# Kernel optimization log

Measured on AMD Instinct MI355X. Metric: run time of the kernel, lower is better.

Reference implementation:

```python
import jax, jax.numpy as jnp
import numpy as np

N, E, B, DIM, NF, EF, HID = 50000, 100000, 2000, 64, 14, 4, 128


def setup_inputs() -> dict:
    key = jax.random.key(0)
    ks = jax.random.split(key, 30)
    rn = lambda k, shape, scale: jax.random.normal(k, shape, jnp.float32) * scale
    inp = {}
    inp["x"] = rn(ks[0], (N, NF), 1.0)
    inp["edge_attr"] = jax.random.uniform(ks[1], (E, EF), jnp.float32)
    inp["edge_index"] = jax.random.randint(ks[2], (2, E), 0, N)
    # equal-size graphs: 25 nodes per graph, sorted segment ids
    inp["batch"] = (jnp.arange(N, dtype=jnp.int32) // (N // B)).astype(jnp.int32)
    inp["lin0_w"] = rn(ks[3], (DIM, NF), (1.0 / NF) ** 0.5)
    inp["lin0_b"] = jnp.zeros((DIM,), jnp.float32)
    inp["mlp_w1"] = rn(ks[4], (HID, EF), (1.0 / EF) ** 0.5)
    inp["mlp_b1"] = jnp.zeros((HID,), jnp.float32)
    inp["mlp_w2"] = rn(ks[5], (DIM * DIM, HID), (1.0 / HID) ** 0.5)
    inp["mlp_b2"] = jnp.zeros((DIM * DIM,), jnp.float32)
    inp["root"] = rn(ks[6], (DIM, DIM), (1.0 / DIM) ** 0.5)
    inp["conv_b"] = jnp.zeros((DIM,), jnp.float32)
    inp["gru_wih"] = rn(ks[7], (3 * DIM, DIM), (1.0 / DIM) ** 0.5)
    inp["gru_whh"] = rn(ks[8], (3 * DIM, DIM), (1.0 / DIM) ** 0.5)
    inp["gru_bih"] = jnp.zeros((3 * DIM,), jnp.float32)
    inp["gru_bhh"] = jnp.zeros((3 * DIM,), jnp.float32)
    inp["lstm_wih"] = rn(ks[9], (4 * DIM, 2 * DIM), (1.0 / (2 * DIM)) ** 0.5)
    inp["lstm_whh"] = rn(ks[10], (4 * DIM, DIM), (1.0 / DIM) ** 0.5)
    inp["lstm_bih"] = jnp.zeros((4 * DIM,), jnp.float32)
    inp["lstm_bhh"] = jnp.zeros((4 * DIM,), jnp.float32)
    inp["lin1_w"] = rn(ks[11], (DIM, 2 * DIM), (1.0 / (2 * DIM)) ** 0.5)
    inp["lin1_b"] = jnp.zeros((DIM,), jnp.float32)
    inp["lin2_w"] = rn(ks[12], (1, DIM), (1.0 / DIM) ** 0.5)
    inp["lin2_b"] = jnp.zeros((1,), jnp.float32)
    return inp


def _forward(x, edge_attr, edge_index, batch, lin0_w, lin0_b, mlp_w1, mlp_b1,
             mlp_w2, mlp_b2, root, conv_b, gru_wih, gru_whh, gru_bih, gru_bhh,
             lstm_wih, lstm_whh, lstm_bih, lstm_bhh, lin1_w, lin1_b, lin2_w, lin2_b):
    src, dst = edge_index[0], edge_index[1]
    n = x.shape[0]
    # edge MLP -> per-edge weight matrices [E, DIM, DIM]
    h_e = jax.nn.relu(edge_attr @ mlp_w1.T + mlp_b1)
    W_e = (h_e @ mlp_w2.T + mlp_b2).reshape(-1, DIM, DIM)
    deg = jnp.clip(jax.ops.segment_sum(jnp.ones_like(dst, jnp.float32), dst, n), 1.0)

    out = jax.nn.relu(x @ lin0_w.T + lin0_b)
    h = out  # GRU hidden (seq_len=1, 1 layer)
    for _ in range(3):
        msg = jnp.einsum('ei,eio->eo', out[src], W_e)  # per-edge matmul
        agg = jax.ops.segment_sum(msg, dst, n) / deg[:, None]  # scatter-mean
        m = jax.nn.relu(agg + out @ root + conv_b)  # NNConv: aggr + root + bias
        # GRU step
        gi = m @ gru_wih.T + gru_bih
        gh = h @ gru_whh.T + gru_bhh
        i_r, i_z, i_n = jnp.split(gi, 3, axis=-1)
        h_r, h_z, h_n = jnp.split(gh, 3, axis=-1)
        r = jax.nn.sigmoid(i_r + h_r)
        z = jax.nn.sigmoid(i_z + h_z)
        ng = jnp.tanh(i_n + r * h_n)
        h = (1.0 - z) * ng + z * h
        out = h

    # Set2Set pooling, 3 processing steps
    b = B
    qh = jnp.zeros((b, DIM), out.dtype)
    qc = jnp.zeros((b, DIM), out.dtype)
    q_star = jnp.zeros((b, 2 * DIM), out.dtype)
    for _ in range(3):
        gates = q_star @ lstm_wih.T + lstm_bih + qh @ lstm_whh.T + lstm_bhh
        gi_, gf_, gg_, go_ = jnp.split(gates, 4, axis=-1)
        qc = jax.nn.sigmoid(gf_) * qc + jax.nn.sigmoid(gi_) * jnp.tanh(gg_)
        qh = jax.nn.sigmoid(go_) * jnp.tanh(qc)
        q = qh
        e = jnp.sum(out * q[batch], axis=-1)  # [N]
        e_max = jax.ops.segment_max(e, batch, b)
        a = jnp.exp(e - e_max[batch])
        denom = jax.ops.segment_sum(a, batch, b)
        a = a / denom[batch]
        r_read = jax.ops.segment_sum(a[:, None] * out, batch, b)
        q_star = jnp.concatenate([q, r_read], axis=-1)

    y = jax.nn.relu(q_star @ lin1_w.T + lin1_b)
    y = y @ lin2_w.T + lin2_b
    return y.reshape(-1)


def reference(x, edge_attr, edge_index, batch, lin0_w, lin0_b, mlp_w1, mlp_b1,
              mlp_w2, mlp_b2, root, conv_b, gru_wih, gru_whh, gru_bih, gru_bhh,
              lstm_wih, lstm_whh, lstm_bih, lstm_bhh, lin1_w, lin1_b, lin2_w, lin2_b):
    return _forward(x, edge_attr, edge_index, batch, lin0_w, lin0_b, mlp_w1, mlp_b1,
                    mlp_w2, mlp_b2, root, conv_b, gru_wih, gru_whh, gru_bih, gru_bhh,
                    lstm_wih, lstm_whh, lstm_bih, lstm_bhh, lin1_w, lin1_b, lin2_w, lin2_b)
```

## Files before the change

kernel.cpp:

```cpp
#include <hip/hip_runtime.h>
#include <hip/hip_bf16.h>

#define NN 50000
#define EE 100000
#define BB 2000
#define DIM 64
#define NF 14
#define EF 4
#define HID 128
#define EPAD 100096

typedef __attribute__((ext_vector_type(8))) _Float16 half8;
typedef __attribute__((ext_vector_type(4))) _Float16 half4;
typedef __attribute__((ext_vector_type(4))) float floatx4;

__global__ void transpose_kernel(const float* __restrict__ lih, const float* __restrict__ lhh,
                                 const float* __restrict__ l1,
                                 float* __restrict__ lihT, float* __restrict__ lhhT,
                                 float* __restrict__ l1T) {
    int t = blockIdx.x * 256 + threadIdx.x;
    if (t < 256 * 128) { int j = t / 128, k = t % 128; lihT[k * 256 + j] = lih[t]; }
    if (t < 256 * 64) { int j = t / 64, k = t % 64; lhhT[k * 256 + j] = lhh[t]; }
    if (t < 64 * 128) { int d = t / 128, k = t % 128; l1T[k * 64 + d] = l1[t]; }
}

__global__ void prep_gru_kernel(const float* __restrict__ root, const float* __restrict__ b2,
                                const float* __restrict__ wih, const float* __restrict__ whh,
                                const float* __restrict__ bih, const float* __restrict__ bhh,
                                _Float16* __restrict__ W1h, _Float16* __restrict__ W2h,
                                float* __restrict__ fbias) {
    int t = blockIdx.x * 256 + threadIdx.x;
    if (t < 64 * 128) {
        int n = t >> 7, k = t & 127;
        W1h[t] = (_Float16)(k < 64 ? root[k * 64 + n] : b2[(size_t)(k - 64) * 64 + n]);
    }
    if (t < 256 * 128) {
        int n2 = t >> 7, k = t & 127;
        int g = n2 >> 6, j = n2 & 63;
        float v;
        if (g == 0)      v = (k < 64) ? wih[j * 64 + k]         : whh[j * 64 + (k - 64)];
        else if (g == 1) v = (k < 64) ? wih[(64 + j) * 64 + k]  : whh[(64 + j) * 64 + (k - 64)];
        else if (g == 2) v = (k < 64) ? wih[(128 + j) * 64 + k] : 0.f;
        else             v = (k < 64) ? 0.f                     : whh[(128 + j) * 64 + (k - 64)];
        W2h[t] = (_Float16)v;
    }
    if (t < 256) {
        int g = t >> 6, j = t & 63;
        float v = (g == 0) ? bih[j] + bhh[j]
                : (g == 1) ? bih[64 + j] + bhh[64 + j]
                : (g == 2) ? bih[128 + j] : bhh[128 + j];
        fbias[t] = v;
    }
}

__global__ void lin0_kernel(const float* __restrict__ x, const float* __restrict__ w,
                            const float* __restrict__ b, float* __restrict__ hv) {
    int t = blockIdx.x * 256 + threadIdx.x;
    if (t >= NN * 64) return;
    int n = t >> 6, d = t & 63;
    float acc = b[d];
    #pragma unroll
    for (int f = 0; f < NF; f++) acc += x[n * NF + f] * w[d * NF + f];
    hv[t] = fmaxf(acc, 0.f);
}

__global__ void deg_kernel(const int* __restrict__ ei, float* __restrict__ deg) {
    int e = blockIdx.x * 256 + threadIdx.x;
    if (e < EE) atomicAdd(&deg[ei[EE + e]], 1.0f);
}

__global__ void he16_kernel(const float* __restrict__ ea, const float* __restrict__ w1,
                            const float* __restrict__ b1, _Float16* __restrict__ he) {
    int t = blockIdx.x * 256 + threadIdx.x;
    if (t >= EPAD * 128) return;
    int el = t >> 7, h = t & 127;
    float acc = 0.f;
    if (el < EE) {
        const float4 a = *(const float4*)(ea + (size_t)el * 4);
        const float4 w = *(const float4*)(w1 + h * 4);
        acc = fmaxf(b1[h] + a.x * w.x + a.y * w.y + a.z * w.z + a.w * w.w, 0.f);
    }
    he[t] = (_Float16)acc;
}

__global__ void w2rt_kernel(const float* __restrict__ w2, _Float16* __restrict__ W2rT) {
    int t = blockIdx.x * 256 + threadIdx.x;
    if (t >= 64 * 8192) return;
    int o = t >> 13, k = t & 8191, i = k >> 7, h = k & 127;
    W2rT[(size_t)o * 8192 + k] = (_Float16)w2[(size_t)(i * 64 + o) * 128 + h];
}

__global__ __launch_bounds__(256, 2) void msg_gemm_kernel(
    const float* __restrict__ hv, const _Float16* __restrict__ he16,
    const _Float16* __restrict__ W2rT, const int* __restrict__ ei,
    float* __restrict__ agg, float* __restrict__ xsum) {
    __shared__ _Float16 sB[2][16 * 64 * 8];
    __shared__ _Float16 sXs[256 * 68];
    __shared__ int sDst[256];
    const int t = threadIdx.x;
    const int eb = blockIdx.x * 256;
    const int lane = t & 63;
    const int w = t >> 6;
    const int col = lane & 15;
    const int quad = lane >> 4;

    if (t < 256) {
        int e = eb + t;
        sDst[t] = (e < EE) ? ei[EE + e] : 0;
    }
    #pragma unroll 4
    for (int rep = 0; rep < 16; rep++) {
        int idx = rep * 256 + t;
        int el = idx >> 4, d4 = idx & 15;
        int e = eb + el;
        float4 v = {0.f, 0.f, 0.f, 0.f};
        if (e < EE) {
            int src = ei[e];
            v = *(const float4*)(hv + (size_t)src * 64 + d4 * 4);
        }
        half4 h4 = {(_Float16)v.x, (_Float16)v.y, (_Float16)v.z, (_Float16)v.w};
        *(half4*)&sXs[el * 68 + d4 * 4] = h4;
    }

    half8 heReg[4][4];
    #pragma unroll
    for (int mt = 0; mt < 4; mt++) {
        int row = eb + w * 64 + mt * 16 + col;
        #pragma unroll
        for (int p = 0; p < 4; p++)
            heReg[mt][p] = *(const half8*)(he16 + (size_t)row * 128 + p * 32 + quad * 8);
    }

    floatx4 Cacc[4][4];
    #pragma unroll
    for (int mt = 0; mt < 4; mt++)
        #pragma unroll
        for (int nt = 0; nt < 4; nt++)
            Cacc[mt][nt] = (floatx4){0.f, 0.f, 0.f, 0.f};

    const size_t gbase = (size_t)(w * 16 + col) * 8192 + quad * 8;
    half8 pre[4];
    {
        #pragma unroll
        for (int rep = 0; rep < 4; rep++)
            pre[rep] = *(const half8*)(W2rT + gbase + 0 * 128 + rep * 32);
        #pragma unroll
        for (int rep = 0; rep < 4; rep++)
            *(half8*)&sB[0][((w * 4 + rep) * 64 + lane) * 8] = pre[rep];
    }
    __syncthreads();

    #pragma unroll 1
    for (int i = 0; i < 64; i++) {
        int buf = i & 1;
        if (i < 63) {
            #pragma unroll
            for (int rep = 0; rep < 4; rep++)
                pre[rep] = *(const half8*)(W2rT + gbase + (size_t)(i + 1) * 128 + rep * 32);
        }
        _Float16 xsx[4];
        #pragma unroll
        for (int mt = 0; mt < 4; mt++)
            xsx[mt] = sXs[(w * 64 + mt * 16 + col) * 68 + i];
        #pragma unroll
        for (int ks = 0; ks < 4; ks++) {
            half8 bfr[4];
            #pragma unroll
            for (int nt = 0; nt < 4; nt++)
                bfr[nt] = *(const half8*)&sB[buf][((nt * 4 + ks) * 64 + lane) * 8];
            #pragma unroll
            for (int mt = 0; mt < 4; mt++) {
                half8 afr = heReg[mt][ks] * xsx[mt];
                #pragma unroll
                for (int nt = 0; nt < 4; nt++)
                    Cacc[mt][nt] = __builtin_amdgcn_mfma_f32_16x16x32_f16(afr, bfr[nt], Cacc[mt][nt], 0, 0, 0);
            }
        }
        if (i < 63) {
            #pragma unroll
            for (int rep = 0; rep < 4; rep++)
                *(half8*)&sB[buf ^ 1][((w * 4 + rep) * 64 + lane) * 8] = pre[rep];
        }
        __syncthreads();
    }

    #pragma unroll
    for (int mt = 0; mt < 4; mt++) {
        #pragma unroll
        for (int r = 0; r < 4; r++) {
            int el = w * 64 + mt * 16 + quad * 4 + r;
            if (eb + el < EE) {
                float* ap = agg + (size_t)sDst[el] * 64 + col;
                #pragma unroll
                for (int nt = 0; nt < 4; nt++)
                    atomicAdd(ap + nt * 16, Cacc[mt][nt][r]);
            }
        }
    }
    #pragma unroll 4
    for (int rep = 0; rep < 64; rep++) {
        int idx = rep * 256 + t;
        int el = idx >> 6, d = idx & 63;
        if (eb + el < EE)
            atomicAdd(&xsum[(size_t)sDst[el] * 64 + d], (float)sXs[el * 68 + d]);
    }
}

__global__ __launch_bounds__(256, 2) void node_fused_kernel(
    const float* __restrict__ hv_in, float* __restrict__ agg,
    float* __restrict__ xsum, const float* __restrict__ deg,
    const _Float16* __restrict__ W1h, const _Float16* __restrict__ W2h,
    const float* __restrict__ fbias, const float* __restrict__ cb,
    float* __restrict__ hv_out) {
    __shared__ _Float16 sA1[64 * 136];
    __shared__ _Float16 sA2[64 * 136];
    __shared__ float sH[64 * 68];
    __shared__ float sAgg[64 * 68];
    const int t = threadIdx.x;
    const int nb = blockIdx.x * 64;
    const int n = t >> 2, part = t & 3;
    {
        int gn = nb + n;
        bool valid = gn < NN;
        float inv = 1.f;
        if (valid) inv = 1.f / fmaxf(deg[gn], 1.f);
        #pragma unroll
        for (int c4 = 0; c4 < 4; c4++) {
            int d0 = part * 16 + c4 * 4;
            float4 hvv = {0.f, 0.f, 0.f, 0.f}, agv = {0.f, 0.f, 0.f, 0.f}, xsv = {0.f, 0.f, 0.f, 0.f};
            if (valid) {
                hvv = *(const float4*)(hv_in + (size_t)gn * 64 + d0);
                agv = *(const float4*)(agg + (size_t)gn * 64 + d0);
                xsv = *(const float4*)(xsum + (size_t)gn * 64 + d0);
            }
            agv.x *= inv; agv.y *= inv; agv.z *= inv; agv.w *= inv;
            xsv.x *= inv; xsv.y *= inv; xsv.z *= inv; xsv.w *= inv;
            half4 hvh = {(_Float16)hvv.x, (_Float16)hvv.y, (_Float16)hvv.z, (_Float16)hvv.w};
            half4 xsh = {(_Float16)xsv.x, (_Float16)xsv.y, (_Float16)xsv.z, (_Float16)xsv.w};
            *(half4*)&sA1[n * 136 + d0] = hvh;
            *(half4*)&sA1[n * 136 + 64 + d0] = xsh;
            *(half4*)&sA2[n * 136 + 64 + d0] = hvh;
            *(float4*)&sH[n * 68 + d0] = hvv;
            *(float4*)&sAgg[n * 68 + d0] = agv;
        }
        if (valid) {
            float4 z = {0.f, 0.f, 0.f, 0.f};
            #pragma unroll
            for (int c4 = 0; c4 < 4; c4++) {
                int d0 = part * 16 + c4 * 4;
                *(float4*)(agg + (size_t)gn * 64 + d0) = z;
                *(float4*)(xsum + (size_t)gn * 64 + d0) = z;
            }
        }
    }
    __syncthreads();

    const int lane = t & 63, w = t >> 6;
    const int col = lane & 15, quad = lane >> 4;

    floatx4 C1[4];
    #pragma unroll
    for (int nt = 0; nt < 4; nt++) {
        float b = cb[nt * 16 + col];
        C1[nt] = (floatx4){b, b, b, b};
    }
    #pragma unroll
    for (int ks = 0; ks < 4; ks++) {
        half8 a = *(const half8*)&sA1[(w * 16 + col) * 136 + ks * 32 + quad * 8];
        #pragma unroll
        for (int nt = 0; nt < 4; nt++) {
            half8 bfr = *(const half8*)(W1h + (size_t)(nt * 16 + col) * 128 + ks * 32 + quad * 8);
            C1[nt] = __builtin_amdgcn_mfma_f32_16x16x32_f16(a, bfr, C1[nt], 0, 0, 0);
        }
    }
    #pragma unroll
    for (int nt = 0; nt < 4; nt++) {
        #pragma unroll
        for (int r = 0; r < 4; r++) {
            int node = w * 16 + quad * 4 + r;
            int j = nt * 16 + col;
            float m = fmaxf(C1[nt][r] + sAgg[node * 68 + j], 0.f);
            sA2[node * 136 + j] = (_Float16)m;
        }
    }
    __syncthreads();

    floatx4 C2[16];
    #pragma unroll
    for (int nt2 = 0; nt2 < 16; nt2++) {
        float b = fbias[nt2 * 16 + col];
        C2[nt2] = (floatx4){b, b, b, b};
    }
    #pragma unroll
    for (int ks = 0; ks < 4; ks++) {
        half8 a = *(const half8*)&sA2[(w * 16 + col) * 136 + ks * 32 + quad * 8];
        #pragma unroll
        for (int nt2 = 0; nt2 < 16; nt2++) {
            half8 bfr = *(const half8*)(W2h + (size_t)(nt2 * 16 + col) * 128 + ks * 32 + quad * 8);
            C2[nt2] = __builtin_amdgcn_mfma_f32_16x16x32_f16(a, bfr, C2[nt2], 0, 0, 0);
        }
    }
    float hnew[4][4];
    #pragma unroll
    for (int r = 0; r < 4; r++) {
        int node = w * 16 + quad * 4 + r;
        #pragma unroll
        for (int jt = 0; jt < 4; jt++) {
            int j = jt * 16 + col;
            float rr = 1.f / (1.f + expf(-C2[jt][r]));
            float zz = 1.f / (1.f + expf(-C2[4 + jt][r]));
            float ng = tanhf(C2[8 + jt][r] + rr * C2[12 + jt][r]);
            float hold = sH[node * 68 + j];
            hnew[r][jt] = (1.f - zz) * ng + zz * hold;
        }
    }
    __syncthreads();
    #pragma unroll
    for (int r = 0; r < 4; r++) {
        int node = w * 16 + quad * 4 + r;
        #pragma unroll
        for (int jt = 0; jt < 4; jt++)
            sH[node * 68 + jt * 16 + col] = hnew[r][jt];
    }
    __syncthreads();
    {
        int gn = nb + n;
        if (gn < NN) {
            #pragma unroll
            for (int c4 = 0; c4 < 4; c4++) {
                int d0 = part * 16 + c4 * 4;
                *(float4*)(hv_out + (size_t)gn * 64 + d0) = *(const float4*)&sH[n * 68 + d0];
            }
        }
    }
}

__global__ __launch_bounds__(256) void set2set_kernel(
    const float* __restrict__ hv,
    const float* __restrict__ lihT, const float* __restrict__ lhhT,
    const float* __restrict__ l_bih, const float* __restrict__ l_bhh,
    const float* __restrict__ lin1T, const float* __restrict__ lin1_b,
    const float* __restrict__ lin2_w, const float* __restrict__ lin2_b,
    float* __restrict__ out) {
    __shared__ float outS[25 * 65];
    __shared__ float qs[128], qh[64], qc[64], gat[256], ew[32], aw[32], red[64];
    int g = blockIdx.x;
    int t = threadIdx.x;
    for (int p = t; p < 25 * 64; p += 256) {
        int j = p >> 6, i = p & 63;
        outS[j * 65 + i] = hv[(size_t)(g * 25 + j) * 64 + i];
    }
    if (t < 128) qs[t] = 0.f;
    if (t < 64) { qh[t] = 0.f; qc[t] = 0.f; }
    __syncthreads();
    for (int it = 0; it < 3; it++) {
        float acc = l_bih[t] + l_bhh[t];
        for (int k = 0; k < 128; k++) acc += qs[k] * lihT[k * 256 + t];
        for (int k = 0; k < 64; k++) acc += qh[k] * lhhT[k * 256 + t];
        gat[t] = acc;
        __syncthreads();
        if (t < 64) {
            float ig = 1.f / (1.f + expf(-gat[t]));
            float fg = 1.f / (1.f + expf(-gat[64 + t]));
            float gg = tanhf(gat[128 + t]);
            float og = 1.f / (1.f + expf(-gat[192 + t]));
            float c = fg * qc[t] + ig * gg;
            qc[t] = c;
            qh[t] = og * tanhf(c);
        }
        __syncthreads();
        if (t < 25) {
            float e = 0.f;
            for (int i = 0; i < 64; i++) e += outS[t * 65 + i] * qh[i];
            ew[t] = e;
        }
        __syncthreads();
        if (t == 0) {
            float mx = ew[0];
            for (int j = 1; j < 25; j++) mx = fmaxf(mx, ew[j]);
            float s = 0.f;
            for (int j = 0; j < 25; j++) { float a = expf(ew[j] - mx); aw[j] = a; s += a; }
            float inv = 1.f / s;
            for (int j = 0; j < 25; j++) aw[j] *= inv;
        }
        __syncthreads();
        if (t < 64) {
            float r = 0.f;
            for (int j = 0; j < 25; j++) r += aw[j] * outS[j * 65 + t];
            qs[t] = qh[t];
            qs[64 + t] = r;
        }
        __syncthreads();
    }
    if (t < 64) {
        float y1 = lin1_b[t];
        for (int k = 0; k < 128; k++) y1 += qs[k] * lin1T[k * 64 + t];
        y1 = fmaxf(y1, 0.f);
        red[t] = y1 * lin2_w[t];
    }
    __syncthreads();
    if (t == 0) {
        float y = lin2_b[0];
        for (int i = 0; i < 64; i++) y += red[i];
        out[g] = y;
    }
}

extern "C" void kernel_launch(void* const* d_in, const int* in_sizes, int n_in,
                              void* d_out, int out_size, void* d_ws, size_t ws_size,
                              hipStream_t stream) {
    const float* x        = (const float*)d_in[0];
    const float* ea       = (const float*)d_in[1];
    const int*   ei       = (const int*)  d_in[2];
    const float* lin0_w   = (const float*)d_in[4];
    const float* lin0_b   = (const float*)d_in[5];
    const float* mlp_w1   = (const float*)d_in[6];
    const float* mlp_b1   = (const float*)d_in[7];
    const float* mlp_w2   = (const float*)d_in[8];
    const float* mlp_b2   = (const float*)d_in[9];
    const float* root     = (const float*)d_in[10];
    const float* conv_b   = (const float*)d_in[11];
    const float* gru_wih  = (const float*)d_in[12];
    const float* gru_whh  = (const float*)d_in[13];
    const float* gru_bih  = (const float*)d_in[14];
    const float* gru_bhh  = (const float*)d_in[15];
    const float* lstm_wih = (const float*)d_in[16];
    const float* lstm_whh = (const float*)d_in[17];
    const float* lstm_bih = (const float*)d_in[18];
    const float* lstm_bhh = (const float*)d_in[19];
    const float* lin1_w   = (const float*)d_in[20];
    const float* lin1_b   = (const float*)d_in[21];
    const float* lin2_w   = (const float*)d_in[22];
    const float* lin2_b   = (const float*)d_in[23];
    float* out = (float*)d_out;

    char* base = (char*)d_ws;
    size_t off = 0;
    auto carve = [&](size_t bytes) -> void* {
        void* r = base + off;
        off = (off + bytes + 255) & ~(size_t)255;
        return r;
    };
    float* hv   = (float*)carve((size_t)NN * 64 * 4);
    float* agg  = (float*)carve((size_t)NN * 64 * 4);
    float* xsum = (float*)carve((size_t)NN * 64 * 4);
    float* deg  = (float*)carve((size_t)NN * 4);
    float* lihT = (float*)carve(128 * 256 * 4);
    float* lhhT = (float*)carve(64 * 256 * 4);
    float* l1T  = (float*)carve(128 * 64 * 4);
    float* fbias = (float*)carve(256 * 4);
    _Float16* he16 = (_Float16*)carve((size_t)EPAD * 128 * 2);
    _Float16* W2rT = (_Float16*)carve((size_t)64 * 8192 * 2);
    _Float16* W1h  = (_Float16*)carve((size_t)64 * 128 * 2);
    _Float16* W2h  = (_Float16*)carve((size_t)256 * 128 * 2);

    hipMemsetAsync(deg, 0, (size_t)NN * 4, stream);
    hipMemsetAsync(agg, 0, (size_t)NN * 64 * 4 * 2, stream);
    transpose_kernel<<<128, 256, 0, stream>>>(lstm_wih, lstm_whh, lin1_w, lihT, lhhT, l1T);
    prep_gru_kernel<<<128, 256, 0, stream>>>(root, mlp_b2, gru_wih, gru_whh, gru_bih, gru_bhh,
                                             W1h, W2h, fbias);
    lin0_kernel<<<(NN * 64 + 255) / 256, 256, 0, stream>>>(x, lin0_w, lin0_b, hv);
    deg_kernel<<<(EE + 255) / 256, 256, 0, stream>>>(ei, deg);
    he16_kernel<<<(EPAD * 128 + 255) / 256, 256, 0, stream>>>(ea, mlp_w1, mlp_b1, he16);
    w2rt_kernel<<<(64 * 8192 + 255) / 256, 256, 0, stream>>>(mlp_w2, W2rT);

    for (int it = 0; it < 3; it++) {
        msg_gemm_kernel<<<EPAD / 256, 256, 0, stream>>>(hv, he16, W2rT, ei, agg, xsum);
        node_fused_kernel<<<(NN + 63) / 64, 256, 0, stream>>>(hv, agg, xsum, deg,
                                                              W1h, W2h, fbias, conv_b, hv);
    }

    set2set_kernel<<<BB, 256, 0, stream>>>(hv, lihT, lhhT, lstm_bih, lstm_bhh,
                                           l1T, lin1_b, lin2_w, lin2_b, out);
}
```

Before: 763.8 us.

## Retile message GEMM to 64-edge blocks with register-streamed W2 operands

```diff
diff --git a/kernel.cpp b/kernel.cpp
--- a/kernel.cpp
+++ b/kernel.cpp
@@ -90,27 +90,26 @@
     W2rT[(size_t)o * 8192 + k] = (_Float16)w2[(size_t)(i * 64 + o) * 128 + h];
 }
 
-__global__ __launch_bounds__(256, 2) void msg_gemm_kernel(
+__global__ __launch_bounds__(128, 2) void msg_gemm_kernel(
     const float* __restrict__ hv, const _Float16* __restrict__ he16,
     const _Float16* __restrict__ W2rT, const int* __restrict__ ei,
     float* __restrict__ agg, float* __restrict__ xsum) {
-    __shared__ _Float16 sB[2][16 * 64 * 8];
-    __shared__ _Float16 sXs[256 * 68];
-    __shared__ int sDst[256];
+    __shared__ _Float16 sXs[64 * 68];
+    __shared__ int sDst[64];
     const int t = threadIdx.x;
-    const int eb = blockIdx.x * 256;
+    const int eb = blockIdx.x * 64;
     const int lane = t & 63;
     const int w = t >> 6;
     const int col = lane & 15;
     const int quad = lane >> 4;
 
-    if (t < 256) {
+    if (t < 64) {
         int e = eb + t;
         sDst[t] = (e < EE) ? ei[EE + e] : 0;
     }
-    #pragma unroll 4
-    for (int rep = 0; rep < 16; rep++) {
-        int idx = rep * 256 + t;
+    #pragma unroll 2
+    for (int rep = 0; rep < 8; rep++) {
+        int idx = rep * 128 + t;
         int el = idx >> 4, d4 = idx & 15;
         int e = eb + el;
         float4 v = {0.f, 0.f, 0.f, 0.f};
@@ -125,81 +124,70 @@
     half8 heReg[4][4];
     #pragma unroll
     for (int mt = 0; mt < 4; mt++) {
-        int row = eb + w * 64 + mt * 16 + col;
+        int row = eb + mt * 16 + col;
         #pragma unroll
         for (int p = 0; p < 4; p++)
             heReg[mt][p] = *(const half8*)(he16 + (size_t)row * 128 + p * 32 + quad * 8);
     }
 
-    floatx4 Cacc[4][4];
-    #pragma unroll
-    for (int mt = 0; mt < 4; mt++)
-        #pragma unroll
-        for (int nt = 0; nt < 4; nt++)
-            Cacc[mt][nt] = (floatx4){0.f, 0.f, 0.f, 0.f};
-
-    const size_t gbase = (size_t)(w * 16 + col) * 8192 + quad * 8;
-    half8 pre[4];
-    {
-        #pragma unroll
-        for (int rep = 0; rep < 4; rep++)
-            pre[rep] = *(const half8*)(W2rT + gbase + 0 * 128 + rep * 32);
-        #pragma unroll
-        for (int rep = 0; rep < 4; rep++)
-            *(half8*)&sB[0][((w * 4 + rep) * 64 + lane) * 8] = pre[rep];
-    }
-    __syncthreads();
-
-    #pragma unroll 1
-    for (int i = 0; i < 64; i++) {
-        int buf = i & 1;
-        if (i < 63) {
+    floatx4 Cacc[4][2];
+    #pragma unroll
+    for (int mt = 0; mt < 4; mt++) {
+        Cacc[mt][0] = (floatx4){0.f, 0.f, 0.f, 0.f};
+        Cacc[mt][1] = (floatx4){0.f, 0.f, 0.f, 0.f};
+    }
+    __syncthreads();
+
+    const _Float16* pB = W2rT + (size_t)(w * 32 + col) * 8192 + quad * 8;
+
+    half8 bufA[2][4], bufB[2][4];
+    auto LOADB = [&](half8 (&dst)[2][4], int i) {
+        #pragma unroll
+        for (int nt = 0; nt < 2; nt++)
             #pragma unroll
-            for (int rep = 0; rep < 4; rep++)
-                pre[rep] = *(const half8*)(W2rT + gbase + (size_t)(i + 1) * 128 + rep * 32);
-        }
-        _Float16 xsx[4];
+            for (int ks = 0; ks < 4; ks++)
+                dst[nt][ks] = *(const half8*)(pB + (size_t)nt * (16 * 8192) + (size_t)i * 128 + ks * 32);
+    };
+    auto STEP = [&](half8 (&b)[2][4], int i) {
+        _Float16 xs[4];
         #pragma unroll
         for (int mt = 0; mt < 4; mt++)
-            xsx[mt] = sXs[(w * 64 + mt * 16 + col) * 68 + i];
+            xs[mt] = sXs[(mt * 16 + col) * 68 + i];
         #pragma unroll
         for (int ks = 0; ks < 4; ks++) {
-            half8 bfr[4];
-            #pragma unroll
-            for (int nt = 0; nt < 4; nt++)
-                bfr[nt] = *(const half8*)&sB[buf][((nt * 4 + ks) * 64 + lane) * 8];
             #pragma unroll
             for (int mt = 0; mt < 4; mt++) {
-                half8 afr = heReg[mt][ks] * xsx[mt];
-                #pragma unroll
-                for (int nt = 0; nt < 4; nt++)
-                    Cacc[mt][nt] = __builtin_amdgcn_mfma_f32_16x16x32_f16(afr, bfr[nt], Cacc[mt][nt], 0, 0, 0);
+                half8 afr = heReg[mt][ks] * xs[mt];
+                Cacc[mt][0] = __builtin_amdgcn_mfma_f32_16x16x32_f16(afr, b[0][ks], Cacc[mt][0], 0, 0, 0);
+                Cacc[mt][1] = __builtin_amdgcn_mfma_f32_16x16x32_f16(afr, b[1][ks], Cacc[mt][1], 0, 0, 0);
             }
         }
-        if (i < 63) {
-            #pragma unroll
-            for (int rep = 0; rep < 4; rep++)
-                *(half8*)&sB[buf ^ 1][((w * 4 + rep) * 64 + lane) * 8] = pre[rep];
-        }
-        __syncthreads();
+    };
+
+    LOADB(bufA, 0);
+    #pragma unroll 1
+    for (int i = 0; i < 64; i += 2) {
+        LOADB(bufB, i + 1);
+        STEP(bufA, i);
+        if (i + 2 < 64) LOADB(bufA, i + 2);
+        STEP(bufB, i + 1);
     }
 
     #pragma unroll
     for (int mt = 0; mt < 4; mt++) {
         #pragma unroll
         for (int r = 0; r < 4; r++) {
-            int el = w * 64 + mt * 16 + quad * 4 + r;
+            int el = mt * 16 + quad * 4 + r;
             if (eb + el < EE) {
-                float* ap = agg + (size_t)sDst[el] * 64 + col;
-                #pragma unroll
-                for (int nt = 0; nt < 4; nt++)
-                    atomicAdd(ap + nt * 16, Cacc[mt][nt][r]);
+                float* ap = agg + (size_t)sDst[el] * 64 + w * 32 + col;
+                atomicAdd(ap, Cacc[mt][0][r]);
+                atomicAdd(ap + 16, Cacc[mt][1][r]);
             }
         }
     }
     #pragma unroll 4
-    for (int rep = 0; rep < 64; rep++) {
-        int idx = rep * 256 + t;
+    for (int rep = 0; rep < 32; rep++) {
+        int idx = rep * 128 + t;
         int el = idx >> 6, d = idx & 63;
         if (eb + el < EE)
             atomicAdd(&xsum[(size_t)sDst[el] * 64 + d], (float)sXs[el * 68 + d]);
@@ -465,7 +453,7 @@
     w2rt_kernel<<<(64 * 8192 + 255) / 256, 256, 0, stream>>>(mlp_w2, W2rT);
 
     for (int it = 0; it < 3; it++) {
-        msg_gemm_kernel<<<EPAD / 256, 256, 0, stream>>>(hv, he16, W2rT, ei, agg, xsum);
+        msg_gemm_kernel<<<(EE + 63) / 64, 128, 0, stream>>>(hv, he16, W2rT, ei, agg, xsum);
         node_fused_kernel<<<(NN + 63) / 64, 256, 0, stream>>>(hv, agg, xsum, deg,
                                                               W1h, W2h, fbias, conv_b, hv);
     }
```

Result: slower. 1.072 ms (+40.3%).

## Switch edge message GEMM to 32x32x16 MFMA with 2x2 wave tiling

Applied to the files above, without the earlier changes.

```diff
diff --git a/kernel.cpp b/kernel.cpp
--- a/kernel.cpp
+++ b/kernel.cpp
@@ -13,6 +13,7 @@
 typedef __attribute__((ext_vector_type(8))) _Float16 half8;
 typedef __attribute__((ext_vector_type(4))) _Float16 half4;
 typedef __attribute__((ext_vector_type(4))) float floatx4;
+typedef __attribute__((ext_vector_type(16))) float floatx16;
 
 __global__ void transpose_kernel(const float* __restrict__ lih, const float* __restrict__ lhh,
                                  const float* __restrict__ l1,
@@ -101,8 +102,10 @@
     const int eb = blockIdx.x * 256;
     const int lane = t & 63;
     const int w = t >> 6;
-    const int col = lane & 15;
-    const int quad = lane >> 4;
+    const int wm = w >> 1;
+    const int wn = w & 1;
+    const int l31 = lane & 31;
+    const int kh = lane >> 5;
 
     if (t < 256) {
         int e = eb + t;
@@ -122,33 +125,41 @@
         *(half4*)&sXs[el * 68 + d4 * 4] = h4;
     }
 
-    half8 heReg[4][4];
+    half8 heReg[4][8];
     #pragma unroll
     for (int mt = 0; mt < 4; mt++) {
-        int row = eb + w * 64 + mt * 16 + col;
-        #pragma unroll
-        for (int p = 0; p < 4; p++)
-            heReg[mt][p] = *(const half8*)(he16 + (size_t)row * 128 + p * 32 + quad * 8);
-    }
-
-    floatx4 Cacc[4][4];
+        int row = eb + wm * 128 + mt * 32 + l31;
+        #pragma unroll
+        for (int s = 0; s < 8; s++)
+            heReg[mt][s] = *(const half8*)(he16 + (size_t)row * 128 + s * 16 + kh * 8);
+    }
+
+    floatx16 Cacc[4];
     #pragma unroll
     for (int mt = 0; mt < 4; mt++)
         #pragma unroll
-        for (int nt = 0; nt < 4; nt++)
-            Cacc[mt][nt] = (floatx4){0.f, 0.f, 0.f, 0.f};
-
-    const size_t gbase = (size_t)(w * 16 + col) * 8192 + quad * 8;
+        for (int r = 0; r < 16; r++) Cacc[mt][r] = 0.f;
+
+    const int f0 = w * 4;
+    const _Float16* gB[4];
+    int wOff[4];
+    #pragma unroll
+    for (int rep = 0; rep < 4; rep++) {
+        int f = f0 + rep;
+        int wnf = f >> 3, sf = f & 7;
+        gB[rep] = W2rT + (size_t)(wnf * 32 + l31) * 8192 + sf * 16 + kh * 8;
+        wOff[rep] = f * 512 + lane * 8;
+    }
     half8 pre[4];
     {
         #pragma unroll
-        for (int rep = 0; rep < 4; rep++)
-            pre[rep] = *(const half8*)(W2rT + gbase + 0 * 128 + rep * 32);
-        #pragma unroll
-        for (int rep = 0; rep < 4; rep++)
-            *(half8*)&sB[0][((w * 4 + rep) * 64 + lane) * 8] = pre[rep];
-    }
-    __syncthreads();
+        for (int rep = 0; rep < 4; rep++) pre[rep] = *(const half8*)(gB[rep]);
+        #pragma unroll
+        for (int rep = 0; rep < 4; rep++) *(half8*)&sB[0][wOff[rep]] = pre[rep];
+    }
+    __syncthreads();
+
+    const int rBase = wn * 4096 + lane * 8;
 
     #pragma unroll 1
     for (int i = 0; i < 64; i++) {
@@ -156,30 +167,25 @@
         if (i < 63) {
             #pragma unroll
             for (int rep = 0; rep < 4; rep++)
-                pre[rep] = *(const half8*)(W2rT + gbase + (size_t)(i + 1) * 128 + rep * 32);
-        }
-        _Float16 xsx[4];
+                pre[rep] = *(const half8*)(gB[rep] + (size_t)(i + 1) * 128);
+        }
+        _Float16 xs[4];
         #pragma unroll
         for (int mt = 0; mt < 4; mt++)
-            xsx[mt] = sXs[(w * 64 + mt * 16 + col) * 68 + i];
-        #pragma unroll
-        for (int ks = 0; ks < 4; ks++) {
-            half8 bfr[4];
-            #pragma unroll
-            for (int nt = 0; nt < 4; nt++)
-                bfr[nt] = *(const half8*)&sB[buf][((nt * 4 + ks) * 64 + lane) * 8];
+            xs[mt] = sXs[(wm * 128 + mt * 32 + l31) * 68 + i];
+        #pragma unroll
+        for (int s = 0; s < 8; s++) {
+            half8 bfr = *(const half8*)&sB[buf][rBase + s * 512];
             #pragma unroll
             for (int mt = 0; mt < 4; mt++) {
-                half8 afr = heReg[mt][ks] * xsx[mt];
-                #pragma unroll
-                for (int nt = 0; nt < 4; nt++)
-                    Cacc[mt][nt] = __builtin_amdgcn_mfma_f32_16x16x32_f16(afr, bfr[nt], Cacc[mt][nt], 0, 0, 0);
+                half8 afr = heReg[mt][s] * xs[mt];
+                Cacc[mt] = __builtin_amdgcn_mfma_f32_32x32x16_f16(afr, bfr, Cacc[mt], 0, 0, 0);
             }
         }
         if (i < 63) {
             #pragma unroll
             for (int rep = 0; rep < 4; rep++)
-                *(half8*)&sB[buf ^ 1][((w * 4 + rep) * 64 + lane) * 8] = pre[rep];
+                *(half8*)&sB[buf ^ 1][wOff[rep]] = pre[rep];
         }
         __syncthreads();
     }
@@ -187,14 +193,11 @@
     #pragma unroll
     for (int mt = 0; mt < 4; mt++) {
         #pragma unroll
-        for (int r = 0; r < 4; r++) {
-            int el = w * 64 + mt * 16 + quad * 4 + r;
-            if (eb + el < EE) {
-                float* ap = agg + (size_t)sDst[el] * 64 + col;
-                #pragma unroll
-                for (int nt = 0; nt < 4; nt++)
-                    atomicAdd(ap + nt * 16, Cacc[mt][nt][r]);
-            }
+        for (int r = 0; r < 16; r++) {
+            int m = (r & 3) + 8 * (r >> 2) + 4 * kh;
+            int el = wm * 128 + mt * 32 + m;
+            if (eb + el < EE)
+                atomicAdd(agg + (size_t)sDst[el] * 64 + wn * 32 + l31, Cacc[mt][r]);
         }
     }
     #pragma unroll 4
```

New measurement: 781.4 us. +2.3%, slower.

## Load message-GEMM B fragments directly from global into registers, dropping LDS staging

Applied to the files above, without the earlier changes.

```diff
diff --git a/kernel.cpp b/kernel.cpp
--- a/kernel.cpp
+++ b/kernel.cpp
@@ -94,7 +94,6 @@
     const float* __restrict__ hv, const _Float16* __restrict__ he16,
     const _Float16* __restrict__ W2rT, const int* __restrict__ ei,
     float* __restrict__ agg, float* __restrict__ xsum) {
-    __shared__ _Float16 sB[2][16 * 64 * 8];
     __shared__ _Float16 sXs[256 * 68];
     __shared__ int sDst[256];
     const int t = threadIdx.x;
@@ -138,50 +137,43 @@
         for (int nt = 0; nt < 4; nt++)
             Cacc[mt][nt] = (floatx4){0.f, 0.f, 0.f, 0.f};
 
-    const size_t gbase = (size_t)(w * 16 + col) * 8192 + quad * 8;
-    half8 pre[4];
-    {
-        #pragma unroll
-        for (int rep = 0; rep < 4; rep++)
-            pre[rep] = *(const half8*)(W2rT + gbase + 0 * 128 + rep * 32);
-        #pragma unroll
-        for (int rep = 0; rep < 4; rep++)
-            *(half8*)&sB[0][((w * 4 + rep) * 64 + lane) * 8] = pre[rep];
-    }
-    __syncthreads();
-
+    __syncthreads();
+
+    const _Float16* pB = W2rT + (size_t)col * 8192 + quad * 8;
+
+    half8 B0[4][2], B1[4][2];
+    auto LOADK = [&](half8 (&dst)[4][2], int i, int ksb) {
+        #pragma unroll
+        for (int nt = 0; nt < 4; nt++)
+            #pragma unroll
+            for (int kl = 0; kl < 2; kl++)
+                dst[nt][kl] = *(const half8*)(pB + (size_t)nt * (16 * 8192)
+                                              + (size_t)i * 128 + (ksb + kl) * 32);
+    };
+    auto HALF = [&](half8 (&b)[4][2], const _Float16 (&xsx)[4], int ksb) {
+        #pragma unroll
+        for (int kl = 0; kl < 2; kl++) {
+            #pragma unroll
+            for (int mt = 0; mt < 4; mt++) {
+                half8 afr = heReg[mt][ksb + kl] * xsx[mt];
+                #pragma unroll
+                for (int nt = 0; nt < 4; nt++)
+                    Cacc[mt][nt] = __builtin_amdgcn_mfma_f32_16x16x32_f16(afr, b[nt][kl], Cacc[mt][nt], 0, 0, 0);
+            }
+        }
+    };
+
+    LOADK(B0, 0, 0);
     #pragma unroll 1
     for (int i = 0; i < 64; i++) {
-        int buf = i & 1;
-        if (i < 63) {
-            #pragma unroll
-            for (int rep = 0; rep < 4; rep++)
-                pre[rep] = *(const half8*)(W2rT + gbase + (size_t)(i + 1) * 128 + rep * 32);
-        }
+        LOADK(B1, i, 2);
         _Float16 xsx[4];
         #pragma unroll
         for (int mt = 0; mt < 4; mt++)
             xsx[mt] = sXs[(w * 64 + mt * 16 + col) * 68 + i];
-        #pragma unroll
-        for (int ks = 0; ks < 4; ks++) {
-            half8 bfr[4];
-            #pragma unroll
-            for (int nt = 0; nt < 4; nt++)
-                bfr[nt] = *(const half8*)&sB[buf][((nt * 4 + ks) * 64 + lane) * 8];
-            #pragma unroll
-            for (int mt = 0; mt < 4; mt++) {
-                half8 afr = heReg[mt][ks] * xsx[mt];
-                #pragma unroll
-                for (int nt = 0; nt < 4; nt++)
-                    Cacc[mt][nt] = __builtin_amdgcn_mfma_f32_16x16x32_f16(afr, bfr[nt], Cacc[mt][nt], 0, 0, 0);
-            }
-        }
-        if (i < 63) {
-            #pragma unroll
-            for (int rep = 0; rep < 4; rep++)
-                *(half8*)&sB[buf ^ 1][((w * 4 + rep) * 64 + lane) * 8] = pre[rep];
-        }
-        __syncthreads();
+        HALF(B0, xsx, 0);
+        if (i < 63) LOADK(B0, i + 1, 0);
+        HALF(B1, xsx, 2);
     }
 
     #pragma unroll
```

After: 1.162 ms. 52.1% more time.
